# Optimization experiments

Hardware: AMD Instinct MI355X
Metric: run time of the kernel (lower is better)

Reference implementation:

```python
import jax, jax.numpy as jnp
import numpy as np


def setup_inputs() -> dict:
    key = jax.random.key(0)
    B, C, L = 32, 512, 4096
    inputs = jax.random.normal(key, (B, C, L), dtype=jnp.float32)
    return {"inputs": inputs, "top_k": 8}


def reference(inputs, top_k):
    # inputs: [B, C, L]. Select top_k values along last dim, keep original order.
    _, top_idxs = jax.lax.top_k(inputs, top_k)          # [B, C, k] indices of k largest
    sorted_idxs = jnp.sort(top_idxs, axis=2)            # restore positional order
    return jnp.take_along_axis(inputs, sorted_idxs, axis=2)  # [B, C, k]
```

## Files before the change

kernel.cpp:

```cpp
#include <hip/hip_runtime.h>
#include <cstdint>

#define ROW_LEN 4096
#define KSEL 8
#define NT 256
#define EPT 16
#define C0 2.30f
#define CANDCAP 128

__device__ inline unsigned ordkey(float f) {
    int t = __float_as_int(f);
    return (unsigned)(t ^ ((t >> 31) | 0x80000000));
}
__device__ inline float unkey(unsigned u) {
    int t = (int)u;
    return __int_as_float(t < 0 ? (t ^ 0x80000000) : ~t);
}

__global__ __launch_bounds__(NT) void kmax_kernel(const float* __restrict__ in,
                                                  float* __restrict__ out) {
    const int row  = blockIdx.x;
    const int tid  = threadIdx.x;
    const int lane = tid & 63;
    const int wave = tid >> 6;

    __shared__ float    cand[CANDCAP];
    __shared__ int      scnt;
    __shared__ unsigned swsum[4];

    if (tid == 0) scnt = 0;

    const float4* p4 = reinterpret_cast<const float4*>(in + (size_t)row * ROW_LEN + (size_t)tid * EPT);
    float k[EPT];
#pragma unroll
    for (int j = 0; j < 4; ++j) {
        float4 a = p4[j];
        k[j * 4 + 0] = a.x;
        k[j * 4 + 1] = a.y;
        k[j * 4 + 2] = a.z;
        k[j * 4 + 3] = a.w;
    }
    __syncthreads();

#pragma unroll
    for (int s = 0; s < EPT; ++s) {
        if (k[s] > C0) {
            int pos = atomicAdd(&scnt, 1);
            if (pos < CANDCAP) cand[pos] = k[s];
        }
    }
    __syncthreads();

    const int cnt = scnt;
    unsigned Tkey;
    if (cnt >= KSEL && cnt <= CANDCAP) {
        float f0 = cand[lane];
        float f1 = cand[lane + 64];
        unsigned c0 = (lane      < cnt) ? ordkey(f0) : 0u;
        unsigned c1 = (lane + 64 < cnt) ? ordkey(f1) : 0u;
        unsigned T = 0;
#pragma unroll
        for (int b = 31; b >= 0; --b) {
            unsigned c = T | (1u << b);
            int n = __popcll(__ballot(c0 >= c)) + __popcll(__ballot(c1 >= c));
            if (n >= KSEL) T = c;
        }
        Tkey = T;
    } else {
        unsigned kk[EPT];
#pragma unroll
        for (int s = 0; s < EPT; ++s) kk[s] = ordkey(k[s]);
        unsigned T = 0;
        for (int b = 31; b >= 0; --b) {
            unsigned c = T | (1u << b);
            int n = 0;
#pragma unroll
            for (int s = 0; s < EPT; ++s) n += __popcll(__ballot(kk[s] >= c));
            if (lane == 0) swsum[wave] = (unsigned)n;
            __syncthreads();
            n = (int)(swsum[0] + swsum[1] + swsum[2] + swsum[3]);
            __syncthreads();
            if (n >= KSEL) T = c;
        }
        Tkey = T;
    }
    const float T = unkey(Tkey);

    int cgt = 0, ceq = 0;
#pragma unroll
    for (int s = 0; s < EPT; ++s) {
        cgt += (k[s] > T);
        ceq += (k[s] == T);
    }
    const unsigned long long lt = (1ull << lane) - 1ull;
    int exGt = 0, totGt = 0;
#pragma unroll
    for (int b = 0; b < 3; ++b) {
        unsigned long long m = __ballot((cgt >> b) & 1);
        exGt  += __popcll(m & lt) << b;
        totGt += __popcll(m) << b;
    }
    int exEq = 0, totEq = 0;
#pragma unroll
    for (int b = 0; b < 5; ++b) {
        unsigned long long m = __ballot((ceq >> b) & 1);
        exEq  += __popcll(m & lt) << b;
        totEq += __popcll(m) << b;
    }
    if (lane == 0) swsum[wave] = ((unsigned)totGt << 16) | (unsigned)totEq;
    __syncthreads();
    unsigned base = 0, tot = 0;
#pragma unroll
    for (int w = 0; w < 4; ++w) {
        unsigned v = swsum[w];
        tot += v;
        if (w < wave) base += v;
    }
    const int totgt = (int)(tot >> 16), toteq = (int)(tot & 0xFFFFu);
    const int pgt = (int)(base >> 16) + exGt;
    const int peq = (int)(base & 0xFFFFu) + exEq;
    const int Q = KSEL - totgt;
    const int mybase = pgt + (peq < Q ? peq : Q);
    float* op = out + (size_t)row * KSEL + mybase;

    if (totgt + toteq == KSEL) {
#pragma unroll
        for (int s = 0; s < EPT; ++s) {
            if (k[s] >= T) { *op++ = k[s]; }
        }
    } else {
        int myq = Q - peq; myq = myq < 0 ? 0 : myq;
        int eqSeen = 0;
#pragma unroll
        for (int s = 0; s < EPT; ++s) {
            bool iseq = (k[s] == T);
            bool sel  = (k[s] > T) || (iseq && (eqSeen < myq));
            eqSeen += iseq;
            if (sel) { *op++ = k[s]; }
        }
    }
}

extern "C" void kernel_launch(void* const* d_in, const int* in_sizes, int n_in,
                              void* d_out, int out_size, void* d_ws, size_t ws_size,
                              hipStream_t stream) {
    const float* in  = (const float*)d_in[0];
    float*       out = (float*)d_out;
    const int rows = in_sizes[0] / ROW_LEN;
    kmax_kernel<<<rows, NT, 0, stream>>>(in, out);
}
```

Measured before the change: 354.2 us.

## Coalesce row loads, use per-wave ballot compaction, and sort selected outputs by index

Each thread now loads float4s strided by the block width, so a wave's loads are fully coalesced instead of each thread reading a contiguous 64-byte chunk. The shared-memory atomic candidate append is replaced by per-wave ballot prefix compaction into 32-slot wave buckets, and the fast-path radix search starts with its top bits preset. Output is built by atomically gathering the 8 selected values with their global indices into shared memory, then one thread sorts them with a network and writes two float4s. Tie handling now uses a binary search over global index, which adds extra barriers in the rare tie case. Overflowing a per-wave cap of 32 forces the slow path more often than the old cap of 128 for the whole block.

Measured after the change: 358.4 us. Within noise of the previous version (+1.2%).

```diff
diff --git a/kernel.cpp b/kernel.cpp
--- a/kernel.cpp
+++ b/kernel.cpp
@@ -6,7 +6,7 @@
 #define NT 256
 #define EPT 16
 #define C0 2.30f
-#define CANDCAP 128
+#define WCAP 32
 
 __device__ inline unsigned ordkey(float f) {
     int t = __float_as_int(f);
@@ -23,59 +23,73 @@
     const int tid  = threadIdx.x;
     const int lane = tid & 63;
     const int wave = tid >> 6;
+    const unsigned long long lt = (1ull << lane) - 1ull;
 
-    __shared__ float    cand[CANDCAP];
-    __shared__ int      scnt;
+    __shared__ float    cand[4 * WCAP];
+    __shared__ unsigned wcnt[4];
     __shared__ unsigned swsum[4];
+    __shared__ float    selV[KSEL];
+    __shared__ int      selGi[KSEL];
+    __shared__ int      selCnt;
 
-    if (tid == 0) scnt = 0;
-
-    const float4* p4 = reinterpret_cast<const float4*>(in + (size_t)row * ROW_LEN + (size_t)tid * EPT);
+    const float4* p4 = reinterpret_cast<const float4*>(in + (size_t)row * ROW_LEN);
     float k[EPT];
 #pragma unroll
     for (int j = 0; j < 4; ++j) {
-        float4 a = p4[j];
-        k[j * 4 + 0] = a.x;
-        k[j * 4 + 1] = a.y;
-        k[j * 4 + 2] = a.z;
-        k[j * 4 + 3] = a.w;
+        float4 a = p4[j * NT + tid];
+        k[j * 4 + 0] = a.x; k[j * 4 + 1] = a.y;
+        k[j * 4 + 2] = a.z; k[j * 4 + 3] = a.w;
     }
+    if (tid == 0) selCnt = 0;
+
+    int off = 0;
+#pragma unroll
+    for (int s = 0; s < EPT; ++s) {
+        bool f = k[s] > C0;
+        unsigned long long m = __ballot(f);
+        if (f) {
+            int pos = off + __popcll(m & lt);
+            if (pos < WCAP) cand[wave * WCAP + pos] = k[s];
+        }
+        off += __popcll(m);
+    }
+    if (lane == 0) wcnt[wave] = (unsigned)off;
     __syncthreads();
 
-#pragma unroll
-    for (int s = 0; s < EPT; ++s) {
-        if (k[s] > C0) {
-            int pos = atomicAdd(&scnt, 1);
-            if (pos < CANDCAP) cand[pos] = k[s];
-        }
-    }
-    __syncthreads();
+    const unsigned w0 = wcnt[0], w1 = wcnt[1], w2 = wcnt[2], w3 = wcnt[3];
+    const unsigned total = w0 + w1 + w2 + w3;
+    const bool fastok = (w0 <= WCAP) && (w1 <= WCAP) && (w2 <= WCAP) &&
+                        (w3 <= WCAP) && (total >= KSEL);
 
-    const int cnt = scnt;
     unsigned Tkey;
-    if (cnt >= KSEL && cnt <= CANDCAP) {
+    int n_gt, n_eq;
+    if (fastok) {
         float f0 = cand[lane];
         float f1 = cand[lane + 64];
-        unsigned c0 = (lane      < cnt) ? ordkey(f0) : 0u;
-        unsigned c1 = (lane + 64 < cnt) ? ordkey(f1) : 0u;
-        unsigned T = 0;
+        bool  v0 = (lane & 31) < wcnt[lane >> 5];
+        bool  v1 = (lane & 31) < wcnt[2 + (lane >> 5)];
+        unsigned c0 = v0 ? ordkey(f0) : 0u;
+        unsigned c1 = v1 ? ordkey(f1) : 0u;
+        unsigned T = 0xC0000000u;
 #pragma unroll
-        for (int b = 31; b >= 0; --b) {
+        for (int b = 29; b >= 0; --b) {
             unsigned c = T | (1u << b);
             int n = __popcll(__ballot(c0 >= c)) + __popcll(__ballot(c1 >= c));
             if (n >= KSEL) T = c;
         }
         Tkey = T;
+        n_gt = __popcll(__ballot(c0 > T)) + __popcll(__ballot(c1 > T));
+        n_eq = __popcll(__ballot(c0 == T)) + __popcll(__ballot(c1 == T));
     } else {
-        unsigned kk[EPT];
+        unsigned ku[EPT];
 #pragma unroll
-        for (int s = 0; s < EPT; ++s) kk[s] = ordkey(k[s]);
-        unsigned T = 0;
+        for (int s = 0; s < EPT; ++s) ku[s] = ordkey(k[s]);
+        unsigned T = 0u;
         for (int b = 31; b >= 0; --b) {
             unsigned c = T | (1u << b);
             int n = 0;
 #pragma unroll
-            for (int s = 0; s < EPT; ++s) n += __popcll(__ballot(kk[s] >= c));
+            for (int s = 0; s < EPT; ++s) n += __popcll(__ballot(ku[s] >= c));
             if (lane == 0) swsum[wave] = (unsigned)n;
             __syncthreads();
             n = (int)(swsum[0] + swsum[1] + swsum[2] + swsum[3]);
@@ -83,61 +97,71 @@
             if (n >= KSEL) T = c;
         }
         Tkey = T;
+        int g = 0, e = 0;
+#pragma unroll
+        for (int s = 0; s < EPT; ++s) {
+            g += __popcll(__ballot(ku[s] > T));
+            e += __popcll(__ballot(ku[s] == T));
+        }
+        if (lane == 0) swsum[wave] = ((unsigned)g << 16) | (unsigned)e;
+        __syncthreads();
+        unsigned tt = swsum[0] + swsum[1] + swsum[2] + swsum[3];
+        __syncthreads();
+        n_gt = (int)(tt >> 16);
+        n_eq = (int)(tt & 0xFFFFu);
     }
-    const float T = unkey(Tkey);
 
-    int cgt = 0, ceq = 0;
+    const float Tf = unkey(Tkey);
+    const int   Q  = KSEL - n_gt;
+    int X;
+    if (n_eq == Q) {
+        X = ROW_LEN;
+    } else {
+        int Xl = 0;
+        for (int b = 11; b >= 0; --b) {
+            int c = Xl | (1 << b);
+            int n = 0;
+#pragma unroll
+            for (int s = 0; s < EPT; ++s) {
+                int gi = (tid << 2) + (((s >> 2) << 10) | (s & 3));
+                n += __popcll(__ballot(k[s] == Tf && gi < c));
+            }
+            if (lane == 0) swsum[wave] = (unsigned)n;
+            __syncthreads();
+            n = (int)(swsum[0] + swsum[1] + swsum[2] + swsum[3]);
+            __syncthreads();
+            if (n < Q) Xl = c;
+        }
+        X = Xl;
+    }
+
 #pragma unroll
     for (int s = 0; s < EPT; ++s) {
-        cgt += (k[s] > T);
-        ceq += (k[s] == T);
+        int gi = (tid << 2) + (((s >> 2) << 10) | (s & 3));
+        bool sel = (k[s] > Tf) || (k[s] == Tf && gi <= X);
+        if (sel) {
+            int pos = atomicAdd(&selCnt, 1) & (KSEL - 1);
+            selV[pos]  = k[s];
+            selGi[pos] = gi;
+        }
     }
-    const unsigned long long lt = (1ull << lane) - 1ull;
-    int exGt = 0, totGt = 0;
+    __syncthreads();
+
+    if (tid == 0) {
+        float v[8]; int g[8];
 #pragma unroll
-    for (int b = 0; b < 3; ++b) {
-        unsigned long long m = __ballot((cgt >> b) & 1);
-        exGt  += __popcll(m & lt) << b;
-        totGt += __popcll(m) << b;
-    }
-    int exEq = 0, totEq = 0;
-#pragma unroll
-    for (int b = 0; b < 5; ++b) {
-        unsigned long long m = __ballot((ceq >> b) & 1);
-        exEq  += __popcll(m & lt) << b;
-        totEq += __popcll(m) << b;
-    }
-    if (lane == 0) swsum[wave] = ((unsigned)totGt << 16) | (unsigned)totEq;
-    __syncthreads();
-    unsigned base = 0, tot = 0;
-#pragma unroll
-    for (int w = 0; w < 4; ++w) {
-        unsigned v = swsum[w];
-        tot += v;
-        if (w < wave) base += v;
-    }
-    const int totgt = (int)(tot >> 16), toteq = (int)(tot & 0xFFFFu);
-    const int pgt = (int)(base >> 16) + exGt;
-    const int peq = (int)(base & 0xFFFFu) + exEq;
-    const int Q = KSEL - totgt;
-    const int mybase = pgt + (peq < Q ? peq : Q);
-    float* op = out + (size_t)row * KSEL + mybase;
-
-    if (totgt + toteq == KSEL) {
-#pragma unroll
-        for (int s = 0; s < EPT; ++s) {
-            if (k[s] >= T) { *op++ = k[s]; }
-        }
-    } else {
-        int myq = Q - peq; myq = myq < 0 ? 0 : myq;
-        int eqSeen = 0;
-#pragma unroll
-        for (int s = 0; s < EPT; ++s) {
-            bool iseq = (k[s] == T);
-            bool sel  = (k[s] > T) || (iseq && (eqSeen < myq));
-            eqSeen += iseq;
-            if (sel) { *op++ = k[s]; }
-        }
+        for (int i = 0; i < 8; ++i) { v[i] = selV[i]; g[i] = selGi[i]; }
+#define CSW(i, j) if (g[i] > g[j]) { int tg = g[i]; g[i] = g[j]; g[j] = tg; \
+                                     float tv = v[i]; v[i] = v[j]; v[j] = tv; }
+        CSW(0,1) CSW(2,3) CSW(4,5) CSW(6,7)
+        CSW(0,2) CSW(1,3) CSW(4,6) CSW(5,7)
+        CSW(1,2) CSW(5,6)
+        CSW(0,4) CSW(1,5) CSW(2,6) CSW(3,7)
+        CSW(2,4) CSW(3,5)
+        CSW(1,2) CSW(3,4) CSW(5,6)
+        float4* o4 = reinterpret_cast<float4*>(out + (size_t)row * KSEL);
+        o4[0] = make_float4(v[0], v[1], v[2], v[3]);
+        o4[1] = make_float4(v[4], v[5], v[6], v[7]);
     }
 }
 
```
